# Kernel optimization log

Measured on AMD Instinct MI355X. Metric: run time of the kernel, lower is better.

The kernel has to match this reference:

```python
import jax, jax.numpy as jnp
import numpy as np

K_TOP = 4
NUM_EXPERTS = 8


def _lstm_dir(x, wih, whh, b):
    # x: [B,T,in], wih: [4H,in], whh: [4H,H], b: [4H] (b_ih+b_hh)
    xW = jnp.einsum('bti,gi->btg', x, wih) + b  # [B,T,4H]
    B = x.shape[0]
    H = whh.shape[1]
    init = (jnp.zeros((B, H), x.dtype), jnp.zeros((B, H), x.dtype))

    def step(carry, xt):
        h, c = carry
        g = xt + h @ whh.T
        i, f, gg, o = jnp.split(g, 4, axis=-1)  # torch gate order i,f,g,o
        c = jax.nn.sigmoid(f) * c + jax.nn.sigmoid(i) * jnp.tanh(gg)
        h = jax.nn.sigmoid(o) * jnp.tanh(c)
        return (h, c), h

    _, hs = jax.lax.scan(step, init, jnp.swapaxes(xW, 0, 1))  # [T,B,H]
    return jnp.swapaxes(hs, 0, 1)


def _bidir_layer(x, Wih, Whh, bih, bhh):
    # Wih: [2,4H,in]; dir 0 forward, dir 1 backward
    hf = _lstm_dir(x, Wih[0], Whh[0], bih[0] + bhh[0])
    hb = _lstm_dir(x[:, ::-1], Wih[1], Whh[1], bih[1] + bhh[1])[:, ::-1]
    return jnp.concatenate([hf, hb], axis=-1)  # [B,T,2H]


def _expert(x, Wih0, Whh0, bih0, bhh0, Wih1, Whh1, bih1, bhh1):
    h = _bidir_layer(x, Wih0, Whh0, bih0, bhh0)   # [B,T,2H]
    h = _bidir_layer(h, Wih1, Whh1, bih1, bhh1)   # [B,T,2H]
    return h


def _cv_squared(v):
    v = v.astype(jnp.float32)
    return jnp.var(v, ddof=1) / (jnp.mean(v) ** 2 + 1e-10)


def _forward(x, spk, wg_w, wg_b, Wih0, Whh0, bih0, bhh0, Wih1, Whh1, bih1, bhh1, fc1_w, fc1_b, fc_w, fc_b, loss_coef=0.01):
    B, T, _ = x.shape
    # --- top-k gating (eval path: clean logits, no noise) ---
    logits = spk @ wg_w.T + wg_b                      # [B,E]
    top_vals, top_idx = jax.lax.top_k(logits, K_TOP + 1)
    gates_k = jax.nn.softmax(top_vals[:, :K_TOP], axis=-1)
    rows = jnp.arange(B)[:, None]
    gates = jnp.zeros_like(logits).at[rows, top_idx[:, :K_TOP]].set(gates_k)  # [B,E]
    load = (gates > 0).sum(0)
    importance = gates.sum(0)
    loss = (_cv_squared(importance) + _cv_squared(load)) * loss_coef
    # --- run all experts (dense mixture, as in source) ---
    expert_h = jax.vmap(_expert, in_axes=(None, 0, 0, 0, 0, 0, 0, 0, 0))(
        x, Wih0, Whh0, bih0, bhh0, Wih1, Whh1, bih1, bhh1)          # [E,B,T,2H]
    expert_out = jnp.einsum('ebtf,hf->ebth', expert_h, fc1_w) + fc1_b  # [E,B,T,H]
    data_output = jnp.einsum('ebth,be->bth', expert_out, gates)        # [B,T,H]
    out = jnp.einsum('bth,oh->bto', data_output, fc_w) + fc_b          # [B,T,O]
    out = jnp.swapaxes(out, 0, 1)                                      # [T,B,O]
    return out, loss


def setup_inputs() -> dict:
    key = jax.random.key(0)
    ks = jax.random.split(key, 16)
    B, T, D, H, E, O, S = 32, 1024, 128, 128, 8, 44, 256
    s = 0.08  # weight scale to keep LSTM gates in sane range
    return {
        'x': jax.random.normal(ks[0], (B, T, D), jnp.float32),
        'spk': jax.random.normal(ks[1], (B, S), jnp.float32),
        'wg_w': jax.random.normal(ks[2], (E, S), jnp.float32) * s,
        'wg_b': jax.random.normal(ks[3], (E,), jnp.float32) * s,
        'Wih0': jax.random.normal(ks[4], (E, 2, 4 * H, D), jnp.float32) * s,
        'Whh0': jax.random.normal(ks[5], (E, 2, 4 * H, H), jnp.float32) * s,
        'bih0': jax.random.normal(ks[6], (E, 2, 4 * H), jnp.float32) * s,
        'bhh0': jax.random.normal(ks[7], (E, 2, 4 * H), jnp.float32) * s,
        'Wih1': jax.random.normal(ks[8], (E, 2, 4 * H, 2 * H), jnp.float32) * s,
        'Whh1': jax.random.normal(ks[9], (E, 2, 4 * H, H), jnp.float32) * s,
        'bih1': jax.random.normal(ks[10], (E, 2, 4 * H), jnp.float32) * s,
        'bhh1': jax.random.normal(ks[11], (E, 2, 4 * H), jnp.float32) * s,
        'fc1_w': jax.random.normal(ks[12], (H, 2 * H), jnp.float32) * s,
        'fc1_b': jax.random.normal(ks[13], (H,), jnp.float32) * s,
        'fc_w': jax.random.normal(ks[14], (O, H), jnp.float32) * s,
        'fc_b': jax.random.normal(ks[15], (O,), jnp.float32) * s,
    }


def reference(x, spk, wg_w, wg_b, Wih0, Whh0, bih0, bhh0, Wih1, Whh1, bih1, bhh1, fc1_w, fc1_b, fc_w, fc_b):
    return _forward(x, spk, wg_w, wg_b, Wih0, Whh0, bih0, bhh0, Wih1, Whh1, bih1, bhh1, fc1_w, fc1_b, fc_w, fc_b)
```

## Files before the change

### kernel.cpp

```cpp
#include <hip/hip_runtime.h>

typedef __attribute__((ext_vector_type(4))) float f32x4;
typedef __attribute__((ext_vector_type(8))) short s16x8;

#define LOG2E 1.4426950408889634f
#define K2L   2.8853900817779268f

__device__ __forceinline__ unsigned short f2bf(float f) {
  union { float f; unsigned int i; } v; v.f = f;
  unsigned int u = v.i;
  u = (u + 0x7FFFu + ((u >> 16) & 1u)) >> 16;
  return (unsigned short)u;
}
__device__ __forceinline__ float bf2f(unsigned short s) {
  union { unsigned int i; float f; } v; v.i = ((unsigned int)s) << 16;
  return v.f;
}
__device__ __forceinline__ float rcp_(float x) { return __builtin_amdgcn_rcpf(x); }
__device__ __forceinline__ float ex2(float x) { return __builtin_amdgcn_exp2f(x); }
__device__ __forceinline__ f32x4 mfma16(s16x8 a, s16x8 b, f32x4 c) {
  return __builtin_amdgcn_mfma_f32_16x16x32_bf16(a, b, c, 0, 0, 0);
}
__device__ __forceinline__ s16x8 pack8s(const float* s, float sc) {
  s16x8 v;
#pragma unroll
  for (int j = 0; j < 8; ++j) v[j] = (short)f2bf(s[j] * sc);
  return v;
}

#define BARRIER_LGKM() asm volatile("s_waitcnt lgkmcnt(0)\n\ts_barrier" ::: "memory")

#define OFF_H0   0
#define OFF_XW   134217728
#define OFF_XT   201326592
#define OFF_WHH  209715200
#define OFF_H1C  213909504
#define OFF_HST  230686720
#define OFF_CST  230817792
#define OFF_M    231079936
#define OFF_CV   231129088
#define OFF_G    231129344
#define OFF_WIH0 231130368
#define OFF_WIH1 233227520
#define OFF_BIA  237421824
#define WS_NEED  237552896

__global__ void wsdbg_kernel(float* __restrict__ out, float v) { out[0] = v; }

__global__ void prep_kernel(const float* __restrict__ Whh0, const float* __restrict__ Whh1,
                            const float* __restrict__ Wih0, const float* __restrict__ Wih1,
                            const float* __restrict__ bih0, const float* __restrict__ bhh0,
                            const float* __restrict__ bih1, const float* __restrict__ bhh1,
                            unsigned short* __restrict__ whhb,
                            unsigned short* __restrict__ wihb0,
                            unsigned short* __restrict__ wihb1,
                            float* __restrict__ biasb) {
  const int tid = blockIdx.x * 512 + threadIdx.x;
  for (int i = tid; i < 5242880; i += 2097152) {
    if (i < 2097152) {
      const int gate = (i >> 14) & 3;
      const float sc = (gate == 2) ? K2L : -LOG2E;
      whhb[i] = f2bf((i < 1048576 ? Whh0[i] : Whh1[i - 1048576]) * sc);
    } else if (i < 3145728) {
      const int j = i - 2097152;
      const int gate = (j >> 14) & 3;
      const float sc = (gate == 2) ? K2L : -LOG2E;
      wihb0[j] = f2bf(Wih0[j] * sc);
    } else {
      const int j = i - 3145728;
      const int gate = (j >> 15) & 3;
      const float sc = (gate == 2) ? K2L : -LOG2E;
      wihb1[j] = f2bf(Wih1[j] * sc);
    }
  }
  if (tid < 16384) {
    const int L = tid >> 13, rem = tid & 8191;
    const int gate = (rem >> 7) & 3;
    const float sc = (gate == 2) ? K2L : -LOG2E;
    const float b = L ? (bih1[rem] + bhh1[rem]) : (bih0[rem] + bhh0[rem]);
    biasb[tid] = b * sc;
  }
}

__global__ void prepx_kernel(const float* __restrict__ x, unsigned short* __restrict__ xt) {
  const int i = blockIdx.x * 512 + threadIdx.x;
  for (int j = i; j < 4194304; j += 2097152) {
    const int b = j >> 17, rem = j & 131071, t = rem >> 7, f = rem & 127;
    xt[((size_t)t * 32 + b) * 128 + f] = f2bf(x[j]);
  }
}

__global__ void mprep_kernel(const float* __restrict__ fc1w, const float* __restrict__ fc1b,
                             const float* __restrict__ fcw, const float* __restrict__ fcb,
                             float* __restrict__ M, float* __restrict__ Cv) {
  const int mi = blockIdx.x * 256 + threadIdx.x;
  if (mi < 12288) {
    const int dd = mi / 6144, rem = mi % 6144, o = rem >> 7, hc = rem & 127;
    float s = 0.f;
    if (o < 44)
      for (int h = 0; h < 128; ++h) s += fcw[o * 128 + h] * fc1w[h * 256 + dd * 128 + hc];
    M[mi] = s;
  }
  if (blockIdx.x == 0 && threadIdx.x < 44) {
    const int o = threadIdx.x;
    float s = fcb[o];
    for (int h = 0; h < 128; ++h) s += fcw[o * 128 + h] * fc1b[h];
    Cv[o] = s;
  }
}

__global__ void initout_kernel(const float* __restrict__ Cv, float* __restrict__ out) {
  const int i = blockIdx.x * 512 + threadIdx.x;
  if (i < 1441792) out[i] = Cv[i % 44];
}

__global__ void gating_kernel(const float* __restrict__ spk,
                              const float* __restrict__ wgw,
                              const float* __restrict__ wgb,
                              float* __restrict__ gates_out,
                              float* __restrict__ loss_out) {
  __shared__ __align__(16) float logits[32][8];
  __shared__ __align__(16) float gmat[32][8];
  const int tid = threadIdx.x;
  {
    const int b = tid >> 3, e = tid & 7;
    float s = wgb[e];
    for (int k = 0; k < 256; ++k) s += spk[b * 256 + k] * wgw[e * 256 + k];
    logits[b][e] = s;
  }
  __syncthreads();
  if (tid < 32) {
    const int b = tid;
    float v[8];
    for (int e = 0; e < 8; ++e) v[e] = logits[b][e];
    int idx[4]; float val[4];
    unsigned used = 0;
    for (int k = 0; k < 4; ++k) {
      float best = -1e30f; int bi = 0;
      for (int e = 0; e < 8; ++e)
        if (!((used >> e) & 1) && v[e] > best) { best = v[e]; bi = e; }
      used |= (1u << bi); idx[k] = bi; val[k] = best;
    }
    const float m = val[0];
    float ex[4], ssum = 0.f;
    for (int k = 0; k < 4; ++k) { ex[k] = ex2(LOG2E * (val[k] - m)); ssum += ex[k]; }
    for (int e = 0; e < 8; ++e) gmat[b][e] = 0.f;
    for (int k = 0; k < 4; ++k) gmat[b][idx[k]] = ex[k] / ssum;
    for (int e = 0; e < 8; ++e) gates_out[b * 8 + e] = gmat[b][e];
  }
  __syncthreads();
  if (tid == 0) {
    float imp[8], ld[8];
    for (int e = 0; e < 8; ++e) {
      float si = 0.f, sl = 0.f;
      for (int b = 0; b < 32; ++b) { si += gmat[b][e]; sl += (gmat[b][e] > 0.f) ? 1.f : 0.f; }
      imp[e] = si; ld[e] = sl;
    }
    float mi = 0.f, ml = 0.f;
    for (int e = 0; e < 8; ++e) { mi += imp[e]; ml += ld[e]; }
    mi *= 0.125f; ml *= 0.125f;
    float vi = 0.f, vl = 0.f;
    for (int e = 0; e < 8; ++e) {
      vi += (imp[e] - mi) * (imp[e] - mi);
      vl += (ld[e] - ml) * (ld[e] - ml);
    }
    vi /= 7.f; vl /= 7.f;
    loss_out[0] = 0.01f * (vi / (mi * mi + 1e-10f) + vl / (ml * ml + 1e-10f));
  }
}

template <int L>
__global__ __launch_bounds__(512, 1) void fused(
    int k,
    const unsigned short* __restrict__ Asrc,
    const unsigned short* __restrict__ wihb,
    const float* __restrict__ biasb,
    const unsigned short* __restrict__ whhb,
    unsigned short* __restrict__ xwbufs,
    unsigned short* __restrict__ hstate, float* __restrict__ cstate,
    unsigned short* __restrict__ hout,
    const float* __restrict__ Mmat, const float* __restrict__ gatesp,
    float* __restrict__ outp) {
  constexpr int KC = L ? 8 : 4;
  constexpr int KS = KC * 32;
  const int tid = threadIdx.x, w = tid >> 6, l = tid & 63;
  const int l15 = l & 15, lq = l >> 4;

  if (L && blockIdx.x >= 192) {
    const int c2 = k - 2;
    if (c2 < 0 || c2 > 15) return;
    if (w >= 6) return;
    const int ss = blockIdx.x - 192;
    const int mt = (w >= 3) ? 1 : 0, ot = w - mt * 3;
    const int o = ot * 16 + l15;
    const bool ov = o < 44;
    s16x8 bfm[2][4];
#pragma unroll
    for (int dd = 0; dd < 2; ++dd)
#pragma unroll
      for (int kc = 0; kc < 4; ++kc) {
        if (ov) bfm[dd][kc] = pack8s(Mmat + ((size_t)dd * 48 + o) * 128 + kc * 32 + lq * 8, 1.f);
        else { s16x8 z = {0,0,0,0,0,0,0,0}; bfm[dd][kc] = z; }
      }
    const unsigned short* hb = hout + (size_t)(c2 & 1) * 4194304;
    f32x4 acc0 = {0.f,0.f,0.f,0.f}, acc1 = {0.f,0.f,0.f,0.f};
    for (int e = 0; e < 8; ++e) {
      const unsigned short* ap = hb + ((((size_t)e * 64 + ss) * 32) + mt * 16 + l15) * 256 + lq * 8;
      f32x4 p0 = {0.f,0.f,0.f,0.f}, p1 = {0.f,0.f,0.f,0.f};
#pragma unroll
      for (int kc = 0; kc < 4; ++kc) {
        s16x8 a0 = *(const s16x8*)(ap + kc * 32);
        s16x8 a1 = *(const s16x8*)(ap + 128 + kc * 32);
        p0 = mfma16(a0, bfm[0][kc], p0);
        p1 = mfma16(a1, bfm[1][kc], p1);
      }
#pragma unroll
      for (int r = 0; r < 4; ++r) {
        const float g = gatesp[(mt * 16 + lq * 4 + r) * 8 + e];
        acc0[r] += g * p0[r];
        acc1[r] += g * p1[r];
      }
    }
    if (ov) {
      const int s2 = c2 * 64 + ss, t1 = 1023 - s2;
#pragma unroll
      for (int r = 0; r < 4; ++r) {
        const int b = mt * 16 + lq * 4 + r;
        outp[((size_t)s2 * 32 + b) * 44 + o] += acc0[r];
        outp[((size_t)t1 * 32 + b) * 44 + o] += acc1[r];
      }
    }
    return;
  }

  if (blockIdx.x >= 32) {
    if (k >= 16) return;
    const int gb = blockIdx.x - 32;
    const int ed = gb & 15, e = ed >> 1, d = ed & 1;
    const int slice = gb >> 4;
    const int nsl = L ? 10 : 14;
    unsigned short* xw = xwbufs + (size_t)(k & 1) * 16777216;

    s16x8 bf[4][KC];
    float bias[4];
#pragma unroll
    for (int j = 0; j < 4; ++j) {
      const int n = w * 64 + j * 16 + l15;
      bias[j] = biasb[ed * 512 + n];
      const unsigned short* wp = wihb + ((size_t)ed * 512 + n) * KS + lq * 8;
#pragma unroll
      for (int kc = 0; kc < KC; ++kc) bf[j][kc] = *(const s16x8*)(wp + kc * 32);
    }
    for (int ss = slice; ss < 64; ss += nsl) {
      const int s = k * 64 + ss;
      const int t = d ? 1023 - s : s;
#pragma unroll
      for (int mt = 0; mt < 2; ++mt) {
        const size_t arow = (size_t)(L ? (e * 1024 + t) : t) * 32 + mt * 16 + l15;
        const unsigned short* ap = Asrc + arow * KS + lq * 8;
        s16x8 af[KC];
#pragma unroll
        for (int kc = 0; kc < KC; ++kc) af[kc] = *(const s16x8*)(ap + kc * 32);
        f32x4 acc[4];
#pragma unroll
        for (int j = 0; j < 4; ++j) acc[j] = f32x4{bias[j], bias[j], bias[j], bias[j]};
#pragma unroll
        for (int kc = 0; kc < KC; ++kc) {
#pragma unroll
          for (int j = 0; j < 4; ++j) acc[j] = mfma16(af[kc], bf[j][kc], acc[j]);
        }
        unsigned short* op = xw + (((size_t)(ed * 2 + mt) * 64 + ss) * 512) * 16 + lq * 4;
#pragma unroll
        for (int j = 0; j < 4; ++j) {
          const int n = w * 64 + j * 16 + l15;
          ushort4 o4;
          o4.x = f2bf(acc[j][0]); o4.y = f2bf(acc[j][1]);
          o4.z = f2bf(acc[j][2]); o4.w = f2bf(acc[j][3]);
          *(ushort4*)(op + (size_t)n * 16) = o4;
        }
      }
    }
    return;
  }

  const int c = k - 1;
  if (c < 0 || c > 15) return;
  const int rb = blockIdx.x, ed2 = rb >> 1, bh = rb & 1;
  const int e = ed2 >> 1, d = ed2 & 1;
  __shared__ __align__(16) char hbf[2][4096];
  const int cell = w * 16 + l15;

  s16x8 bfh[4][4];
#pragma unroll
  for (int g = 0; g < 4; ++g) {
    const unsigned short* wp = whhb + ((size_t)ed2 * 512 + g * 128 + cell) * 128 + lq * 8;
#pragma unroll
    for (int kc = 0; kc < 4; ++kc) bfh[g][kc] = *(const s16x8*)(wp + kc * 32);
  }
  const int wb0 = ((cell >> 5) << 10) | (((cell >> 3) & 3) << 8) | ((cell & 7) << 1);
  float cst[4];
  unsigned short hb4[4];
  if (c == 0) {
#pragma unroll
    for (int r = 0; r < 4; ++r) { cst[r] = 0.f; hb4[r] = 0; }
    if (tid < 256) {
      s16x8 z = {0,0,0,0,0,0,0,0};
      *(s16x8*)(&hbf[0][tid * 16]) = z;
    }
  } else {
    const float* cp = cstate + ((size_t)rb * 512 + tid) * 4;
    const unsigned short* hp = hstate + ((size_t)rb * 512 + tid) * 4;
#pragma unroll
    for (int r = 0; r < 4; ++r) {
      cst[r] = cp[r];
      hb4[r] = hp[r];
      *(unsigned short*)(&hbf[0][wb0 | ((lq * 4 + r) << 4)]) = hp[r];
    }
  }
  __syncthreads();

  const unsigned short* xwb =
      xwbufs + (size_t)(c & 1) * 16777216 + ((size_t)(ed2 * 2 + bh) * 64) * 8192 + cell * 16 + lq * 4;
  const int brow = bh * 16 + lq * 4;

  ushort4 xqA[4], xqB[4];
#pragma unroll
  for (int g = 0; g < 4; ++g) {
    xqA[g] = *(const ushort4*)(xwb + g * 2048);
    xqB[g] = *(const ushort4*)(xwb + 8192 + g * 2048);
  }

  auto step = [&](int tt, ushort4* xq) {
    const int p = tt & 1;
    f32x4 a[4];
#pragma unroll
    for (int g = 0; g < 4; ++g) {
      a[g][0] = bf2f(xq[g].x); a[g][1] = bf2f(xq[g].y);
      a[g][2] = bf2f(xq[g].z); a[g][3] = bf2f(xq[g].w);
    }
    {
      const int tn = tt < 62 ? tt + 2 : 63;
#pragma unroll
      for (int g = 0; g < 4; ++g) xq[g] = *(const ushort4*)(xwb + (size_t)tn * 8192 + g * 2048);
    }
    if (tt > 0) {
      const int ptt = tt - 1;
      size_t ob;
      if (L) {
        ob = (size_t)(c & 1) * 4194304 + (((size_t)e * 64 + ptt) * 32 + brow) * 256 + d * 128 + cell;
      } else {
        const int s = c * 64 + ptt;
        const int tg = d ? 1023 - s : s;
        ob = (((size_t)e * 1024 + tg) * 32 + brow) * 256 + d * 128 + cell;
      }
#pragma unroll
      for (int r = 0; r < 4; ++r) hout[ob + (size_t)r * 256] = hb4[r];
    }
    s16x8 hf[4];
#pragma unroll
    for (int kc = 0; kc < 4; ++kc) hf[kc] = *(const s16x8*)(&hbf[p][kc * 1024 + l * 16]);
#pragma unroll
    for (int kc = 0; kc < 4; ++kc) {
#pragma unroll
      for (int g = 0; g < 4; ++g) a[g] = mfma16(hf[kc], bfh[g][kc], a[g]);
    }
#pragma unroll
    for (int r = 0; r < 4; ++r) {
      const float ai = ex2(fminf(a[0][r], 23.f));
      const float af = ex2(fminf(a[1][r], 23.f));
      const float bg = ex2(fminf(a[2][r], 80.f));
      const float ao = ex2(fminf(a[3][r], 23.f));
      const float pai = 1.f + ai, paf = 1.f + af, pbg = 1.f + bg;
      const float t1 = pai * pbg;
      const float r1 = rcp_(paf * t1);
      const float bgm = __builtin_fmaf(bg, K2L, -K2L);
      const float num = __builtin_fmaf(bgm, paf, cst[r] * t1);
      const float cc = num * r1;
      cst[r] = cc;
      const float qc = ex2(fminf(cc, 80.f));
      const float r2 = rcp_((1.f + ao) * (1.f + qc));
      hb4[r] = f2bf((qc - 1.f) * r2);
    }
    char* hw = &hbf[1 - p][0];
#pragma unroll
    for (int r = 0; r < 4; ++r)
      *(unsigned short*)(hw + (wb0 | ((lq * 4 + r) << 4))) = hb4[r];
    BARRIER_LGKM();
  };

  for (int t2 = 0; t2 < 64; t2 += 2) {
    step(t2, xqA);
    step(t2 + 1, xqB);
  }

  {
    size_t ob;
    if (L) {
      ob = (size_t)(c & 1) * 4194304 + (((size_t)e * 64 + 63) * 32 + brow) * 256 + d * 128 + cell;
    } else {
      const int s = c * 64 + 63;
      const int tg = d ? 1023 - s : s;
      ob = (((size_t)e * 1024 + tg) * 32 + brow) * 256 + d * 128 + cell;
    }
#pragma unroll
    for (int r = 0; r < 4; ++r) hout[ob + (size_t)r * 256] = hb4[r];
    unsigned short* hsp = hstate + ((size_t)rb * 512 + tid) * 4;
    float* csp = cstate + ((size_t)rb * 512 + tid) * 4;
#pragma unroll
    for (int r = 0; r < 4; ++r) { hsp[r] = hb4[r]; csp[r] = cst[r]; }
  }
}

extern "C" void kernel_launch(void* const* d_in, const int* in_sizes, int n_in,
                              void* d_out, int out_size, void* d_ws, size_t ws_size,
                              hipStream_t stream) {
  const float* x    = (const float*)d_in[0];
  const float* spk  = (const float*)d_in[1];
  const float* wgw  = (const float*)d_in[2];
  const float* wgb  = (const float*)d_in[3];
  const float* Wih0 = (const float*)d_in[4];
  const float* Whh0 = (const float*)d_in[5];
  const float* bih0 = (const float*)d_in[6];
  const float* bhh0 = (const float*)d_in[7];
  const float* Wih1 = (const float*)d_in[8];
  const float* Whh1 = (const float*)d_in[9];
  const float* bih1 = (const float*)d_in[10];
  const float* bhh1 = (const float*)d_in[11];
  const float* fc1w = (const float*)d_in[12];
  const float* fc1b = (const float*)d_in[13];
  const float* fcw  = (const float*)d_in[14];
  const float* fcb  = (const float*)d_in[15];
  float* out = (float*)d_out;

  if (ws_size < (size_t)WS_NEED) {
    wsdbg_kernel<<<1, 1, 0, stream>>>(out, (float)(ws_size >> 20));
    return;
  }
  char* ws = (char*)d_ws;
  unsigned short* h0     = (unsigned short*)(ws + OFF_H0);
  unsigned short* xwbufs = (unsigned short*)(ws + OFF_XW);
  unsigned short* xt     = (unsigned short*)(ws + OFF_XT);
  unsigned short* whhb   = (unsigned short*)(ws + OFF_WHH);
  unsigned short* h1c    = (unsigned short*)(ws + OFF_H1C);
  unsigned short* hstate = (unsigned short*)(ws + OFF_HST);
  float*          cstate = (float*)(ws + OFF_CST);
  float*          Mmat   = (float*)(ws + OFF_M);
  float*          Cv     = (float*)(ws + OFF_CV);
  float*          gatesw = (float*)(ws + OFF_G);
  unsigned short* wihb0  = (unsigned short*)(ws + OFF_WIH0);
  unsigned short* wihb1  = (unsigned short*)(ws + OFF_WIH1);
  float*          biasb  = (float*)(ws + OFF_BIA);

  prep_kernel<<<4096, 512, 0, stream>>>(Whh0, Whh1, Wih0, Wih1, bih0, bhh0, bih1, bhh1,
                                        whhb, wihb0, wihb1, biasb);
  prepx_kernel<<<4096, 512, 0, stream>>>(x, xt);
  mprep_kernel<<<48, 256, 0, stream>>>(fc1w, fc1b, fcw, fcb, Mmat, Cv);
  initout_kernel<<<2816, 512, 0, stream>>>(Cv, out);
  gating_kernel<<<1, 256, 0, stream>>>(spk, wgw, wgb, gatesw, out + 1441792);

  for (int k = 0; k <= 16; ++k)
    fused<0><<<256, 512, 0, stream>>>(k, xt, wihb0, biasb, whhb, xwbufs,
                                      hstate, cstate, h0, nullptr, nullptr, out);
  for (int k = 0; k <= 17; ++k)
    fused<1><<<256, 512, 0, stream>>>(k, h0, wihb1, biasb + 8192, whhb + 1048576, xwbufs,
                                      hstate, cstate, h1c, Mmat, gatesw, out);
}
```

Measured before the change: 2.491 ms.

## Simplify LSTM recurrence loop: single-step prefetch, setprio, cheaper gate math

The recurrent LSTM kernel drops the two-step-ahead register double buffer of xW and prefetches only the next timestep into a temporary. It raises wave priority for the recurrence and replaces the custom waitcnt+barrier asm with __syncthreads. The cell update is rewritten to use separate reciprocals for the forget gate and the input*candidate product, and the exp clamps on the i/f/o gates are removed. These changes aim to shorten the serial per-step critical path, but the lighter prefetch may expose global load latency, and the unclamped exponentials rely on rcp of infinity giving zero.

```diff
diff --git a/kernel.cpp b/kernel.cpp
--- a/kernel.cpp
+++ b/kernel.cpp
@@ -27,8 +27,6 @@
   for (int j = 0; j < 8; ++j) v[j] = (short)f2bf(s[j] * sc);
   return v;
 }
-
-#define BARRIER_LGKM() asm volatile("s_waitcnt lgkmcnt(0)\n\ts_barrier" ::: "memory")
 
 #define OFF_H0   0
 #define OFF_XW   134217728
@@ -285,6 +283,7 @@
 
   const int c = k - 1;
   if (c < 0 || c > 15) return;
+  __builtin_amdgcn_s_setprio(2);
   const int rb = blockIdx.x, ed2 = rb >> 1, bh = rb & 1;
   const int e = ed2 >> 1, d = ed2 & 1;
   __shared__ __align__(16) char hbf[2][4096];
@@ -323,25 +322,17 @@
       xwbufs + (size_t)(c & 1) * 16777216 + ((size_t)(ed2 * 2 + bh) * 64) * 8192 + cell * 16 + lq * 4;
   const int brow = bh * 16 + lq * 4;
 
-  ushort4 xqA[4], xqB[4];
-#pragma unroll
-  for (int g = 0; g < 4; ++g) {
-    xqA[g] = *(const ushort4*)(xwb + g * 2048);
-    xqB[g] = *(const ushort4*)(xwb + 8192 + g * 2048);
-  }
-
-  auto step = [&](int tt, ushort4* xq) {
+  ushort4 xq[4];
+#pragma unroll
+  for (int g = 0; g < 4; ++g) xq[g] = *(const ushort4*)(xwb + g * 2048);
+
+  for (int tt = 0; tt < 64; ++tt) {
     const int p = tt & 1;
-    f32x4 a[4];
-#pragma unroll
-    for (int g = 0; g < 4; ++g) {
-      a[g][0] = bf2f(xq[g].x); a[g][1] = bf2f(xq[g].y);
-      a[g][2] = bf2f(xq[g].z); a[g][3] = bf2f(xq[g].w);
-    }
+    ushort4 nxq[4];
     {
-      const int tn = tt < 62 ? tt + 2 : 63;
-#pragma unroll
-      for (int g = 0; g < 4; ++g) xq[g] = *(const ushort4*)(xwb + (size_t)tn * 8192 + g * 2048);
+      const int tn = tt < 63 ? tt + 1 : 63;
+#pragma unroll
+      for (int g = 0; g < 4; ++g) nxq[g] = *(const ushort4*)(xwb + (size_t)tn * 8192 + g * 2048);
     }
     if (tt > 0) {
       const int ptt = tt - 1;
@@ -356,26 +347,32 @@
 #pragma unroll
       for (int r = 0; r < 4; ++r) hout[ob + (size_t)r * 256] = hb4[r];
     }
+
     s16x8 hf[4];
 #pragma unroll
     for (int kc = 0; kc < 4; ++kc) hf[kc] = *(const s16x8*)(&hbf[p][kc * 1024 + l * 16]);
+    f32x4 a[4];
+#pragma unroll
+    for (int g = 0; g < 4; ++g) {
+      a[g][0] = bf2f(xq[g].x); a[g][1] = bf2f(xq[g].y);
+      a[g][2] = bf2f(xq[g].z); a[g][3] = bf2f(xq[g].w);
+    }
 #pragma unroll
     for (int kc = 0; kc < 4; ++kc) {
 #pragma unroll
       for (int g = 0; g < 4; ++g) a[g] = mfma16(hf[kc], bfh[g][kc], a[g]);
     }
+
 #pragma unroll
     for (int r = 0; r < 4; ++r) {
-      const float ai = ex2(fminf(a[0][r], 23.f));
-      const float af = ex2(fminf(a[1][r], 23.f));
+      const float ai = ex2(a[0][r]);
+      const float af = ex2(a[1][r]);
       const float bg = ex2(fminf(a[2][r], 80.f));
-      const float ao = ex2(fminf(a[3][r], 23.f));
-      const float pai = 1.f + ai, paf = 1.f + af, pbg = 1.f + bg;
-      const float t1 = pai * pbg;
-      const float r1 = rcp_(paf * t1);
+      const float ao = ex2(a[3][r]);
+      const float sf = rcp_(1.f + af);
+      const float r1 = rcp_((1.f + ai) * (1.f + bg));
       const float bgm = __builtin_fmaf(bg, K2L, -K2L);
-      const float num = __builtin_fmaf(bgm, paf, cst[r] * t1);
-      const float cc = num * r1;
+      const float cc = __builtin_fmaf(sf, cst[r], bgm * r1);
       cst[r] = cc;
       const float qc = ex2(fminf(cc, 80.f));
       const float r2 = rcp_((1.f + ao) * (1.f + qc));
@@ -385,12 +382,9 @@
 #pragma unroll
     for (int r = 0; r < 4; ++r)
       *(unsigned short*)(hw + (wb0 | ((lq * 4 + r) << 4))) = hb4[r];
-    BARRIER_LGKM();
-  };
-
-  for (int t2 = 0; t2 < 64; t2 += 2) {
-    step(t2, xqA);
-    step(t2 + 1, xqB);
+    __syncthreads();
+#pragma unroll
+    for (int g = 0; g < 4; ++g) xq[g] = nxq[g];
   }
 
   {
@@ -409,6 +403,7 @@
 #pragma unroll
     for (int r = 0; r < 4; ++r) { hsp[r] = hb4[r]; csp[r] = cst[r]; }
   }
+  __builtin_amdgcn_s_setprio(0);
 }
 
 extern "C" void kernel_launch(void* const* d_in, const int* in_sizes, int n_in,
```

Result: faster. 2.060 ms (median of 2 runs) (-17.3%).
